# Optimization experiments

Measured on AMD Instinct MI355X. Metric: run time of the kernel, lower is better.

## Reference

```python
import jax, jax.numpy as jnp
import numpy as np

EMBED_DIM = 1024
N_HEAD = 16
HEAD_DIM = EMBED_DIM // N_HEAD
B, S = 2, 2048


def setup_inputs() -> dict:
    key = jax.random.key(0)
    ks = jax.random.split(key, 11)
    d = EMBED_DIM
    scale = 1.0 / np.sqrt(d)
    inp = {
        "query_inp": jax.random.normal(ks[0], (B, S, d), dtype=jnp.float32),
        "key_inp": jax.random.normal(ks[1], (B, S, d), dtype=jnp.float32),
        "value_inp": jax.random.normal(ks[2], (B, S, d), dtype=jnp.float32),
        "Wq": jax.random.normal(ks[3], (d, d), dtype=jnp.float32) * scale,
        "bq": jnp.zeros((d,), dtype=jnp.float32),
        "Wk": jax.random.normal(ks[4], (d, d), dtype=jnp.float32) * scale,
        "bk": jnp.zeros((d,), dtype=jnp.float32),
        "Wv": jax.random.normal(ks[5], (d, d), dtype=jnp.float32) * scale,
        "bv": jnp.zeros((d,), dtype=jnp.float32),
        "Wo": jax.random.normal(ks[6], (d, d), dtype=jnp.float32) * scale,
        "bo": jnp.zeros((d,), dtype=jnp.float32),
    }
    return inp


def reference(query_inp, key_inp, value_inp, Wq, bq, Wk, bk, Wv, bv, Wo, bo):
    b, s, _ = query_inp.shape
    # Linear projections (weights stored as [in, out]); split heads -> [b, h, s, hd]
    def proj(x, W, bias):
        y = jnp.einsum("bsd,de->bse", x, W) + bias
        return y.reshape(b, s, N_HEAD, HEAD_DIM).transpose(0, 2, 1, 3)

    q = proj(query_inp, Wq, bq)
    k = proj(key_inp, Wk, bk)
    v = proj(value_inp, Wv, bv)

    scores = jnp.einsum("bhqd,bhkd->bhqk", q, k) / jnp.sqrt(
        jnp.asarray(HEAD_DIM, dtype=q.dtype)
    )
    attn = jax.nn.softmax(scores, axis=-1)
    out = jnp.einsum("bhqk,bhkd->bhqd", attn, v)  # [b, h, s, hd]
    out = out.transpose(0, 2, 1, 3).reshape(b, s, EMBED_DIM)
    return jnp.einsum("bsd,de->bse", out, Wo) + bo
```

## Files before the change

### kernel.cpp

```cpp
#include <hip/hip_runtime.h>


typedef __bf16 bf16;
typedef __bf16 bf16x4 __attribute__((ext_vector_type(4)));
typedef __bf16 bf16x8 __attribute__((ext_vector_type(8)));
typedef float f32x4 __attribute__((ext_vector_type(4)));

#define DEV static __device__ __forceinline__

constexpr int D = 1024;
constexpr int NH = 16;
constexpr int HD = 64;
constexpr int B_ = 2;
constexpr int S_ = 2048;
constexpr size_t MAT = (size_t)D * D;
constexpr size_t XSZ = (size_t)B_ * S_ * D;

DEV void glds16(const bf16* g, bf16* l) {
  __builtin_amdgcn_global_load_lds(
      (__attribute__((address_space(1))) void*)g,
      (__attribute__((address_space(3))) void*)l, 16, 0, 0);
}

__global__ __launch_bounds__(256) void detect_k(const unsigned short* __restrict__ w,
                                                int* __restrict__ flag) {
  __shared__ int sbuf[256];
  const int tid = threadIdx.x;
  int cnt = 0;
  for (int i = tid; i < 8192; i += 256) {
    const unsigned e = (w[i] >> 7) & 0xFF;
    if (e >= 0x90) cnt++;
  }
  sbuf[tid] = cnt;
  __syncthreads();
  for (int s = 128; s > 0; s >>= 1) {
    if (tid < s) sbuf[tid] += sbuf[tid + s];
    __syncthreads();
  }
  if (tid == 0) flag[0] = (sbuf[0] > 32) ? 1 : 0;
}

__global__ __launch_bounds__(256) void convert_x(const void* __restrict__ X0,
                                                 const void* __restrict__ X1,
                                                 const void* __restrict__ X2,
                                                 const int* __restrict__ flag,
                                                 bf16* __restrict__ Xc) {
  const int isf = *flag;
  const void* s = (blockIdx.y == 0) ? X0 : (blockIdx.y == 1) ? X1 : X2;
  const size_t vi = (size_t)blockIdx.x * 256 + threadIdx.x;
  bf16* dst = Xc + (size_t)blockIdx.y * XSZ + vi * 4;
  if (isf) {
    const float4 f = ((const float4*)s)[vi];
    bf16x4 o = {(bf16)f.x, (bf16)f.y, (bf16)f.z, (bf16)f.w};
    *(bf16x4*)dst = o;
  } else {
    *(bf16x4*)dst = *(const bf16x4*)((const bf16*)s + vi * 4);
  }
}

__global__ __launch_bounds__(256) void convert_bias(const void* __restrict__ b0,
                                                    const void* __restrict__ b1,
                                                    const void* __restrict__ b2,
                                                    const void* __restrict__ b3,
                                                    const int* __restrict__ flag,
                                                    bf16* __restrict__ bc) {
  const int isf = *flag;
  const int m = blockIdx.x;
  const void* s = (m == 0) ? b0 : (m == 1) ? b1 : (m == 2) ? b2 : b3;
  bf16* dst = bc + m * 1024;
  for (int i = threadIdx.x; i < 1024; i += 256)
    dst[i] = isf ? (bf16)((const float*)s)[i] : ((const bf16*)s)[i];
}

__global__ __launch_bounds__(256) void transpose4(const void* __restrict__ W0,
                                                  const void* __restrict__ W1,
                                                  const void* __restrict__ W2,
                                                  const void* __restrict__ W3,
                                                  const int* __restrict__ flag,
                                                  bf16* __restrict__ out) {
  __shared__ bf16 t[64][65];
  const int isf = *flag;
  const int mat = blockIdx.z;
  const void* W = (mat == 0) ? W0 : (mat == 1) ? W1 : (mat == 2) ? W2 : W3;
  bf16* o = out + (size_t)mat * MAT;
  const int r0 = blockIdx.y * 64, c0 = blockIdx.x * 64;
  const int tt = threadIdx.x;
#pragma unroll
  for (int e = 0; e < 16; e++) {
    const int idx = tt + e * 256;
    const size_t gi = (size_t)(r0 + (idx >> 6)) * D + c0 + (idx & 63);
    t[idx >> 6][idx & 63] = isf ? (bf16)((const float*)W)[gi] : ((const bf16*)W)[gi];
  }
  __syncthreads();
#pragma unroll
  for (int e = 0; e < 16; e++) {
    const int idx = tt + e * 256;
    const int co = idx >> 6, ro = idx & 63;
    o[(size_t)(c0 + co) * D + r0 + ro] = t[ro][co];
  }
}

DEV void gemm_core(const bf16* __restrict__ A, const bf16* __restrict__ WT,
                   int m0, int n0, bf16* As, bf16* Bs, f32x4 acc[4][4]) {
  const int tid = threadIdx.x;
  const int w = tid >> 6, lane = tid & 63;
  const int ln = lane & 15, qd = lane >> 4;
  const int wr = w >> 1, wc = w & 1;
  const int l8r = lane >> 3, l8c = lane & 7;
  const int swz8 = ((l8c ^ l8r) * 8);

#pragma unroll
  for (int i = 0; i < 4; i++)
#pragma unroll
    for (int j = 0; j < 4; j++) acc[i][j] = (f32x4){0.f, 0.f, 0.f, 0.f};

  for (int k0 = 0; k0 < D; k0 += 64) {
    __syncthreads();
#pragma unroll
    for (int t = 0; t < 4; t++) {
      const int c = w * 4 + t;
      glds16(A + (size_t)(m0 + c * 8 + l8r) * D + k0 + swz8, As + c * 512);
      glds16(WT + (size_t)(n0 + c * 8 + l8r) * D + k0 + swz8, Bs + c * 512);
    }
    __syncthreads();
#pragma unroll
    for (int ks = 0; ks < 2; ks++) {
      bf16x8 af[4], bfr[4];
#pragma unroll
      for (int i = 0; i < 4; i++)
        af[i] = *(const bf16x8*)(As + (wr * 64 + i * 16 + ln) * 64 +
                                 (((ks * 4 + qd) ^ (ln & 7)) * 8));
#pragma unroll
      for (int j = 0; j < 4; j++)
        bfr[j] = *(const bf16x8*)(Bs + (wc * 64 + j * 16 + ln) * 64 +
                                  (((ks * 4 + qd) ^ (ln & 7)) * 8));
#pragma unroll
      for (int i = 0; i < 4; i++)
#pragma unroll
        for (int j = 0; j < 4; j++)
          acc[i][j] = __builtin_amdgcn_mfma_f32_16x16x32_bf16(af[i], bfr[j], acc[i][j], 0, 0, 0);
    }
  }
}

__global__ __launch_bounds__(256) void qkv_kernel(
    const bf16* __restrict__ Xc, const bf16* __restrict__ WT4, const bf16* __restrict__ bc,
    bf16* __restrict__ Qb, bf16* __restrict__ Kb, bf16* __restrict__ Vb) {
  __shared__ __align__(16) bf16 As[128 * 64];
  __shared__ __align__(16) bf16 Bs[128 * 64];
  const int mt = blockIdx.x;
  const int nb = blockIdx.y;
  const int mat = nb >> 3;
  const int n0 = (nb & 7) * 128;
  const bf16* A = Xc + (size_t)mat * XSZ;
  const bf16* WT = WT4 + (size_t)mat * MAT;
  const bf16* bias = bc + mat * 1024;

  f32x4 acc[4][4];
  gemm_core(A, WT, mt * 128, n0, As, Bs, acc);

  const int tid = threadIdx.x;
  const int w = tid >> 6, lane = tid & 63;
  const int ln = lane & 15, qd = lane >> 4;
  const int wr = w >> 1, wc = w & 1;
  bf16* dst = (mat == 0) ? Qb : (mat == 1) ? Kb : Vb;
  const float scale = (mat == 0) ? 0.125f : 1.0f;

#pragma unroll
  for (int i = 0; i < 4; i++)
#pragma unroll
    for (int j = 0; j < 4; j++) {
      const int col = n0 + wc * 64 + j * 16 + ln;
      const float bb = (float)bias[col];
      const int h = col >> 6, dd = col & 63;
      const int tok0 = mt * 128 + wr * 64 + i * 16 + qd * 4;
      const int b = tok0 >> 11, s0 = tok0 & (S_ - 1);
      bf16* base = dst + (size_t)(b * NH + h) * S_ * HD;
      if (mat == 2) {
        bf16x4 pv;
#pragma unroll
        for (int r = 0; r < 4; r++) pv[r] = (bf16)(acc[i][j][r] + bb);
        const size_t off = ((size_t)((dd >> 4) * (S_ >> 5) + (s0 >> 5))) * 512 +
                           ((s0 >> 3) & 3) * 128 + (dd & 15) * 8 + (s0 & 7);
        *(bf16x4*)(base + off) = pv;
      } else {
#pragma unroll
        for (int r = 0; r < 4; r++) {
          const int s = s0 + r;
          const size_t off = ((size_t)(s >> 4)) * 1024 + (dd >> 3) * 128 + (s & 15) * 8 + (dd & 7);
          base[off] = (bf16)((acc[i][j][r] + bb) * scale);
        }
      }
    }
}

__global__ __launch_bounds__(256, 3) void attn_kernel(const bf16* __restrict__ Qb,
                                                      const bf16* __restrict__ Kb,
                                                      const bf16* __restrict__ Vb,
                                                      bf16* __restrict__ Opart,
                                                      float2* __restrict__ ml) {
  __shared__ __align__(16) bf16 P2[128 * 136];

  const int bh = blockIdx.x;
  const int qt = blockIdx.y;
  const int sp = blockIdx.z;
  const int tid = threadIdx.x;
  const int w = tid >> 6, lane = tid & 63;
  const int ln = lane & 15, qd = lane >> 4;

  const size_t base = (size_t)bh * S_ * HD;
  const int q0 = qt * 128;
  const bf16* Kp = Kb + base;
  const bf16* Vp = Vb + base;
  const bf16* Qp = Qb + base;
  bf16* Pw = P2 + (w * 32) * 136;

  bf16x8 qf[2][2];
#pragma unroll
  for (int i = 0; i < 2; i++)
#pragma unroll
    for (int t = 0; t < 2; t++)
      qf[i][t] = *(const bf16x8*)(Qp + (size_t)(qt * 8 + w * 2 + i) * 1024 +
                                  (t * 4 + qd) * 128 + ln * 8);

  f32x4 acc_o[2][4];
#pragma unroll
  for (int i = 0; i < 2; i++)
#pragma unroll
    for (int j = 0; j < 4; j++) acc_o[i][j] = (f32x4){0.f, 0.f, 0.f, 0.f};
  float m_i[2] = {-1e30f, -1e30f}, l_i[2] = {0.f, 0.f};

  const int kbeg = sp * (S_ / 2), kend = kbeg + (S_ / 2);
  for (int k0 = kbeg; k0 < kend; k0 += 128) {
    f32x4 st[2][8];
#pragma unroll
    for (int i = 0; i < 2; i++)
#pragma unroll
      for (int j = 0; j < 8; j++) st[i][j] = (f32x4){0.f, 0.f, 0.f, 0.f};
#pragma unroll
    for (int t = 0; t < 2; t++) {
      bf16x8 kf[8];
#pragma unroll
      for (int j = 0; j < 8; j++)
        kf[j] = *(const bf16x8*)(Kp + (size_t)((k0 >> 4) + j) * 1024 +
                                 (t * 4 + qd) * 128 + ln * 8);
#pragma unroll
      for (int i = 0; i < 2; i++)
#pragma unroll
        for (int j = 0; j < 8; j++)
          st[i][j] = __builtin_amdgcn_mfma_f32_16x16x32_bf16(kf[j], qf[i][t], st[i][j], 0, 0, 0);
    }

#pragma unroll
    for (int i = 0; i < 2; i++) {
      float mx = -1e30f;
#pragma unroll
      for (int j = 0; j < 8; j++)
#pragma unroll
        for (int r = 0; r < 4; r++) mx = fmaxf(mx, st[i][j][r]);
      mx = fmaxf(mx, __shfl_xor(mx, 16));
      mx = fmaxf(mx, __shfl_xor(mx, 32));
      const float mnew = fmaxf(m_i[i], mx);
      const float alpha = __expf(m_i[i] - mnew);
      m_i[i] = mnew;
      float rs = 0.f;
#pragma unroll
      for (int j = 0; j < 8; j++)
#pragma unroll
        for (int r = 0; r < 4; r++) {
          const float p = __expf(st[i][j][r] - mnew);
          st[i][j][r] = p;
          rs += p;
        }
      rs += __shfl_xor(rs, 16);
      rs += __shfl_xor(rs, 32);
      l_i[i] = l_i[i] * alpha + rs;

      {
        bf16* pr = Pw + (i * 16 + ln) * 136;
#pragma unroll
        for (int j = 0; j < 8; j++) {
          bf16x4 pv;
#pragma unroll
          for (int r = 0; r < 4; r++) pv[r] = (bf16)st[i][j][r];
          const int c0 = j * 2 + (qd >> 1);
          *(bf16x4*)(pr + ((c0 ^ (ln & 7)) * 8) + (qd & 1) * 4) = pv;
        }
      }

#pragma unroll
      for (int r = 0; r < 4; r++) {
        const float ar = __shfl(alpha, qd * 4 + r);
#pragma unroll
        for (int jn = 0; jn < 4; jn++) acc_o[i][jn][r] *= ar;
      }
    }

#pragma unroll
    for (int t = 0; t < 4; t++) {
      bf16x8 vf[4], pf[2];
#pragma unroll
      for (int jn = 0; jn < 4; jn++)
        vf[jn] = *(const bf16x8*)(Vp + (size_t)(jn * (S_ >> 5) + (k0 >> 5) + t) * 512 +
                                  qd * 128 + ln * 8);
#pragma unroll
      for (int i = 0; i < 2; i++)
        pf[i] = *(const bf16x8*)(Pw + (i * 16 + ln) * 136 + (((t * 4 + qd) ^ (ln & 7)) * 8));
#pragma unroll
      for (int i = 0; i < 2; i++)
#pragma unroll
        for (int jn = 0; jn < 4; jn++)
          acc_o[i][jn] = __builtin_amdgcn_mfma_f32_16x16x32_bf16(pf[i], vf[jn], acc_o[i][jn], 0, 0, 0);
    }
  }

  const size_t obase = ((size_t)sp * 32 + bh) * (size_t)S_ * HD;
#pragma unroll
  for (int i = 0; i < 2; i++) {
#pragma unroll
    for (int r = 0; r < 4; r++) {
      const int q = q0 + w * 32 + i * 16 + qd * 4 + r;
#pragma unroll
      for (int jn = 0; jn < 4; jn++)
        Opart[obase + (size_t)q * HD + jn * 16 + ln] = (bf16)acc_o[i][jn][r];
    }
    if (qd == 0) {
      const int q = q0 + w * 32 + i * 16 + ln;
      ml[((size_t)sp * 32 + bh) * S_ + q] = make_float2(m_i[i], l_i[i]);
    }
  }
}

__global__ __launch_bounds__(256) void merge_k(const bf16* __restrict__ Opart,
                                               const float2* __restrict__ ml,
                                               bf16* __restrict__ Ob) {
  const int gid = blockIdx.x * 256 + threadIdx.x;
  const int dd = gid & 63;
  const int row = gid >> 6;
  const int bh = row >> 11, q = row & 2047;
  const float2 ml0 = ml[row];
  const float2 ml1 = ml[32 * S_ + row];
  const float m = fmaxf(ml0.x, ml1.x);
  const float a0 = __expf(ml0.x - m), a1 = __expf(ml1.x - m);
  const float inv = 1.0f / (a0 * ml0.y + a1 * ml1.y);
  const float o0 = (float)Opart[(size_t)row * HD + dd];
  const float o1 = (float)Opart[((size_t)32 * S_ + row) * HD + dd];
  const int b = bh >> 4, h = bh & 15;
  Ob[((size_t)(b * S_ + q)) * D + h * HD + dd] = (bf16)((a0 * o0 + a1 * o1) * inv);
}

__global__ __launch_bounds__(256) void oproj_kernel(const bf16* __restrict__ Ob,
                                                    const bf16* __restrict__ WoT,
                                                    const bf16* __restrict__ bo,
                                                    const int* __restrict__ flag,
                                                    void* __restrict__ outv) {
  __shared__ __align__(16) bf16 As[128 * 64];
  __shared__ __align__(16) bf16 Bs[128 * 64];
  const int isf = *flag;
  const int mt = blockIdx.x, nb = blockIdx.y;
  f32x4 acc[4][4];
  gemm_core(Ob, WoT, mt * 128, nb * 128, As, Bs, acc);
  const int tid = threadIdx.x;
  const int w = tid >> 6, lane = tid & 63;
  const int ln = lane & 15, qd = lane >> 4;
  const int wr = w >> 1, wc = w & 1;
#pragma unroll
  for (int i = 0; i < 4; i++)
#pragma unroll
    for (int j = 0; j < 4; j++) {
      const int col = nb * 128 + wc * 64 + j * 16 + ln;
      const float bb = (float)bo[col];
#pragma unroll
      for (int r = 0; r < 4; r++) {
        const int tok = mt * 128 + wr * 64 + i * 16 + qd * 4 + r;
        const float v = acc[i][j][r] + bb;
        const size_t oi = (size_t)tok * D + col;
        if (isf) ((float*)outv)[oi] = v;
        else ((bf16*)outv)[oi] = (bf16)v;
      }
    }
}

extern "C" void kernel_launch(void* const* d_in, const int* in_sizes, int n_in,
                              void* d_out, int out_size, void* d_ws, size_t ws_size,
                              hipStream_t stream) {
  int* flag = (int*)d_ws;
  bf16* ws = (bf16*)d_ws + 2048;

  bf16* WT4 = ws;
  bf16* Xc  = WT4 + 4 * MAT;
  bf16* bc  = Xc + 3 * XSZ;
  bf16* Qb  = bc + 4096;
  bf16* Kb  = Qb + XSZ;
  bf16* Vb  = Kb + XSZ;
  bf16* Ob  = Vb + XSZ;
  bf16*   Opart = Xc;
  float2* mlbuf = (float2*)(Xc + 2 * 32 * (size_t)S_ * HD);

  detect_k<<<1, 256, 0, stream>>>((const unsigned short*)d_in[3], flag);
  convert_x<<<dim3(4096, 3), 256, 0, stream>>>(d_in[0], d_in[1], d_in[2], flag, Xc);
  convert_bias<<<4, 256, 0, stream>>>(d_in[4], d_in[6], d_in[8], d_in[10], flag, bc);
  transpose4<<<dim3(16, 16, 4), 256, 0, stream>>>(d_in[3], d_in[5], d_in[7], d_in[9], flag, WT4);
  qkv_kernel<<<dim3(32, 24), 256, 0, stream>>>(Xc, WT4, bc, Qb, Kb, Vb);
  attn_kernel<<<dim3(32, 16, 2), 256, 0, stream>>>(Qb, Kb, Vb, Opart, mlbuf);
  merge_k<<<16384, 256, 0, stream>>>(Opart, mlbuf, Ob);
  oproj_kernel<<<dim3(32, 8), 256, 0, stream>>>(Ob, WT4 + 3 * MAT, bc + 3 * 1024, flag, d_out);
}
```

Measured before the change: 291.5 us.

## Use exp2 softmax, shrink P tile LDS, raise attention occupancy, pack partial outputs

Folds log2(e) into the Q scale so the softmax can use exp2f directly, including in the merge kernel. Shrinks the P staging buffer from 136 to 128 columns with a rotation-based swizzle, and raises the attention kernel's launch-bounds occupancy hint from 3 to 4 blocks per CU. Partial attention outputs are written as packed 4-element vectors in an MFMA-native tile layout, and the merge kernel gathers them through that layout. The aims are less LDS per block, more resident waves, and cheaper exp and store instructions, at the cost of possible register pressure and a less coalesced read pattern in the merge.

```diff
diff --git a/kernel.cpp b/kernel.cpp
--- a/kernel.cpp
+++ b/kernel.cpp
@@ -164,7 +164,7 @@
   const int ln = lane & 15, qd = lane >> 4;
   const int wr = w >> 1, wc = w & 1;
   bf16* dst = (mat == 0) ? Qb : (mat == 1) ? Kb : Vb;
-  const float scale = (mat == 0) ? 0.125f : 1.0f;
+  const float scale = (mat == 0) ? 0.180336880f : 1.0f;
 
 #pragma unroll
   for (int i = 0; i < 4; i++)
@@ -194,12 +194,12 @@
     }
 }
 
-__global__ __launch_bounds__(256, 3) void attn_kernel(const bf16* __restrict__ Qb,
+__global__ __launch_bounds__(256, 4) void attn_kernel(const bf16* __restrict__ Qb,
                                                       const bf16* __restrict__ Kb,
                                                       const bf16* __restrict__ Vb,
                                                       bf16* __restrict__ Opart,
                                                       float2* __restrict__ ml) {
-  __shared__ __align__(16) bf16 P2[128 * 136];
+  __shared__ __align__(16) bf16 P2[128 * 128];
 
   const int bh = blockIdx.x;
   const int qt = blockIdx.y;
@@ -213,7 +213,7 @@
   const bf16* Kp = Kb + base;
   const bf16* Vp = Vb + base;
   const bf16* Qp = Qb + base;
-  bf16* Pw = P2 + (w * 32) * 136;
+  bf16* Pw = P2 + (w * 32) * 128;
 
   bf16x8 qf[2][2];
 #pragma unroll
@@ -261,14 +261,14 @@
       mx = fmaxf(mx, __shfl_xor(mx, 16));
       mx = fmaxf(mx, __shfl_xor(mx, 32));
       const float mnew = fmaxf(m_i[i], mx);
-      const float alpha = __expf(m_i[i] - mnew);
+      const float alpha = exp2f(m_i[i] - mnew);
       m_i[i] = mnew;
       float rs = 0.f;
 #pragma unroll
       for (int j = 0; j < 8; j++)
 #pragma unroll
         for (int r = 0; r < 4; r++) {
-          const float p = __expf(st[i][j][r] - mnew);
+          const float p = exp2f(st[i][j][r] - mnew);
           st[i][j][r] = p;
           rs += p;
         }
@@ -277,14 +277,14 @@
       l_i[i] = l_i[i] * alpha + rs;
 
       {
-        bf16* pr = Pw + (i * 16 + ln) * 136;
+        bf16* pr = Pw + (i * 16 + ln) * 128;
 #pragma unroll
         for (int j = 0; j < 8; j++) {
           bf16x4 pv;
 #pragma unroll
           for (int r = 0; r < 4; r++) pv[r] = (bf16)st[i][j][r];
           const int c0 = j * 2 + (qd >> 1);
-          *(bf16x4*)(pr + ((c0 ^ (ln & 7)) * 8) + (qd & 1) * 4) = pv;
+          *(bf16x4*)(pr + (((c0 + ln) & 15) * 8) + (qd & 1) * 4) = pv;
         }
       }
 
@@ -305,7 +305,7 @@
                                   qd * 128 + ln * 8);
 #pragma unroll
       for (int i = 0; i < 2; i++)
-        pf[i] = *(const bf16x8*)(Pw + (i * 16 + ln) * 136 + (((t * 4 + qd) ^ (ln & 7)) * 8));
+        pf[i] = *(const bf16x8*)(Pw + (i * 16 + ln) * 128 + (((t * 4 + qd + ln) & 15) * 8));
 #pragma unroll
       for (int i = 0; i < 2; i++)
 #pragma unroll
@@ -314,15 +314,16 @@
     }
   }
 
-  const size_t obase = ((size_t)sp * 32 + bh) * (size_t)S_ * HD;
+  const size_t tile = (((size_t)sp * 32 + bh) * 16 + qt) * 4 + w;
+  bf16* ob = Opart + tile * 2048;
 #pragma unroll
   for (int i = 0; i < 2; i++) {
 #pragma unroll
-    for (int r = 0; r < 4; r++) {
-      const int q = q0 + w * 32 + i * 16 + qd * 4 + r;
-#pragma unroll
-      for (int jn = 0; jn < 4; jn++)
-        Opart[obase + (size_t)q * HD + jn * 16 + ln] = (bf16)acc_o[i][jn][r];
+    for (int jn = 0; jn < 4; jn++) {
+      bf16x4 pk;
+#pragma unroll
+      for (int r = 0; r < 4; r++) pk[r] = (bf16)acc_o[i][jn][r];
+      *(bf16x4*)(ob + ((i * 4 + jn) * 64 + lane) * 4) = pk;
     }
     if (qd == 0) {
       const int q = q0 + w * 32 + i * 16 + ln;
@@ -338,13 +339,17 @@
   const int dd = gid & 63;
   const int row = gid >> 6;
   const int bh = row >> 11, q = row & 2047;
+  const int qt = q >> 7, w = (q >> 5) & 3, ii = (q >> 4) & 1, qd = (q >> 2) & 3, r = q & 3;
+  const int jn = dd >> 4, ln = dd & 15;
+  const size_t t0 = ((((size_t)bh * 16 + qt) * 4 + w) * 2048) +
+                    ((ii * 4 + jn) * 64 + qd * 16 + ln) * 4 + r;
   const float2 ml0 = ml[row];
   const float2 ml1 = ml[32 * S_ + row];
   const float m = fmaxf(ml0.x, ml1.x);
-  const float a0 = __expf(ml0.x - m), a1 = __expf(ml1.x - m);
+  const float a0 = exp2f(ml0.x - m), a1 = exp2f(ml1.x - m);
   const float inv = 1.0f / (a0 * ml0.y + a1 * ml1.y);
-  const float o0 = (float)Opart[(size_t)row * HD + dd];
-  const float o1 = (float)Opart[((size_t)32 * S_ + row) * HD + dd];
+  const float o0 = (float)Opart[t0];
+  const float o1 = (float)Opart[XSZ + t0];
   const int b = bh >> 4, h = bh & 15;
   Ob[((size_t)(b * S_ + q)) * D + h * HD + dd] = (bf16)((a0 * o0 + a1 * o1) * inv);
 }
@@ -395,7 +400,7 @@
   bf16* Vb  = Kb + XSZ;
   bf16* Ob  = Vb + XSZ;
   bf16*   Opart = Xc;
-  float2* mlbuf = (float2*)(Xc + 2 * 32 * (size_t)S_ * HD);
+  float2* mlbuf = (float2*)(Xc + 2 * XSZ);
 
   detect_k<<<1, 256, 0, stream>>>((const unsigned short*)d_in[3], flag);
   convert_x<<<dim3(4096, 3), 256, 0, stream>>>(d_in[0], d_in[1], d_in[2], flag, Xc);
```

Measured after the change: 357.6 us. 22.7% more time.
